# Optimization experiments

Measured on AMD Instinct MI355X. Metric: run time of the kernel, lower is better.

The kernel has to match this reference:

```python
import jax, jax.numpy as jnp
import numpy as np

B, N, D = 4, 512, 128
TAU = 0.5
EPS = 1e-9

def setup_inputs() -> dict:
    key = jax.random.key(0)
    ks = jax.random.split(key, 6)
    sc = 0.05  # weight scale for numerical sanity
    return {
        "entity_states": jax.random.normal(ks[0], (B, N, D), dtype=jnp.float32),
        "Wp": jax.random.normal(ks[1], (D, D), dtype=jnp.float32) * sc,
        "bp": jnp.zeros((D,), dtype=jnp.float32),
        "edge_logits": jax.random.normal(ks[2], (N, N), dtype=jnp.float32),
        "W1": jax.random.normal(ks[3], (2 * D, D), dtype=jnp.float32) * sc,
        "b1": jnp.zeros((D,), dtype=jnp.float32),
        "W2": jax.random.normal(ks[4], (D, D), dtype=jnp.float32) * sc,
        "b2": jnp.zeros((D,), dtype=jnp.float32),
        "u_noise": jax.random.uniform(ks[5], (N, N), dtype=jnp.float32),
    }

def reference(entity_states, Wp, bp, edge_logits, W1, b1, W2, b2, u_noise):
    b, n, d = entity_states.shape
    # entity projection
    proj = entity_states @ Wp + bp  # (B,N,D)
    # gumbel-softmax adjacency (row-wise softmax over sources)
    g = -jnp.log(-jnp.log(u_noise + EPS) + EPS)
    A = jax.nn.softmax((edge_logits + g) / TAU, axis=-1)  # (N,N)
    # split concat-MLP first layer: combined = [source_j, target_i]
    W1_src, W1_tgt = W1[:d], W1[d:]
    s = proj @ W1_src  # (B,N,D) contribution of source j
    t = proj @ W1_tgt  # (B,N,D) contribution of target i
    # h[b,i,j,:] = relu(s[b,j] + t[b,i] + b1)
    h = jax.nn.relu(s[:, None, :, :] + t[:, :, None, :] + b1)  # (B,N,N,D)
    msg = h @ W2 + b2  # (B,N,N,D)
    # weighted aggregation over sources j with A[i,j]
    upd = jnp.einsum('ij,bijd->bid', A, msg)  # (B,N,D)
    next_state = entity_states + upd
    return next_state, jnp.broadcast_to(A, (b, n, n))
```

## Files before the change

### kernel.cpp

```cpp
#include <hip/hip_runtime.h>
#include <math.h>

#define Bv 4
#define Nv 512
#define Dv 128
#define BND (Bv*Nv*Dv)
#define NN  (Nv*Nv)
#define EPSv 1e-9f

__global__ __launch_bounds__(256) void k_gumbel_softmax(
    const float* __restrict__ edge_logits,
    const float* __restrict__ u_noise,
    float* __restrict__ A_out)
{
    __shared__ float sred[4];
    const int row = blockIdx.x;
    const int t = threadIdx.x;

    const float u0 = u_noise[row*Nv + t];
    const float u1 = u_noise[row*Nv + t + 256];
    const float g0 = -logf(-logf(u0 + EPSv) + EPSv);
    const float g1 = -logf(-logf(u1 + EPSv) + EPSv);
    const float z0 = (edge_logits[row*Nv + t]       + g0) * 2.0f;
    const float z1 = (edge_logits[row*Nv + t + 256] + g1) * 2.0f;

    float m = fmaxf(z0, z1);
    #pragma unroll
    for (int off = 32; off >= 1; off >>= 1)
        m = fmaxf(m, __shfl_xor(m, off, 64));
    if ((t & 63) == 0) sred[t >> 6] = m;
    __syncthreads();
    m = fmaxf(fmaxf(sred[0], sred[1]), fmaxf(sred[2], sred[3]));

    const float e0 = expf(z0 - m);
    const float e1 = expf(z1 - m);
    float ssum = e0 + e1;
    #pragma unroll
    for (int off = 32; off >= 1; off >>= 1)
        ssum += __shfl_xor(ssum, off, 64);
    __syncthreads();
    if ((t & 63) == 0) sred[t >> 6] = ssum;
    __syncthreads();
    const float inv = 1.0f / (sred[0] + sred[1] + sred[2] + sred[3]);

    const float a0 = e0 * inv;
    const float a1 = e1 * inv;
    #pragma unroll
    for (int bb = 0; bb < Bv; ++bb) {
        A_out[bb*NN + row*Nv + t]       = a0;
        A_out[bb*NN + row*Nv + t + 256] = a1;
    }
}

__global__ __launch_bounds__(256) void k_proj_st(
    const float* __restrict__ ES, const float* __restrict__ Wp,
    const float* __restrict__ bp, const float* __restrict__ W1,
    const float* __restrict__ b1,
    float* __restrict__ s_out, float* __restrict__ t_out)
{
    __shared__ float es[8][Dv];
    __shared__ float pr[8][Dv];
    const int row0 = blockIdx.x * 8;
    const int t = threadIdx.x;
    const int c  = t & 127;
    const int rg = t >> 7;

    for (int idx = t; idx < 8*Dv; idx += 256)
        es[idx >> 7][idx & 127] = ES[(row0 + (idx >> 7))*Dv + (idx & 127)];
    __syncthreads();

    {
        float acc[4];
        const float bpc = bp[c];
        #pragma unroll
        for (int r = 0; r < 4; ++r) acc[r] = bpc;
        for (int k = 0; k < Dv; ++k) {
            const float w = Wp[k*Dv + c];
            #pragma unroll
            for (int r = 0; r < 4; ++r)
                acc[r] = fmaf(es[rg*4 + r][k], w, acc[r]);
        }
        #pragma unroll
        for (int r = 0; r < 4; ++r) pr[rg*4 + r][c] = acc[r];
    }
    __syncthreads();

    float sacc[4], tacc[4];
    const float b1c = b1[c];
    #pragma unroll
    for (int r = 0; r < 4; ++r) { sacc[r] = b1c; tacc[r] = 0.0f; }
    for (int k = 0; k < Dv; ++k) {
        const float ws_ = W1[k*Dv + c];
        const float wt_ = W1[(Dv + k)*Dv + c];
        #pragma unroll
        for (int r = 0; r < 4; ++r) {
            const float pv = pr[rg*4 + r][k];
            sacc[r] = fmaf(pv, ws_, sacc[r]);
            tacc[r] = fmaf(pv, wt_, tacc[r]);
        }
    }
    #pragma unroll
    for (int r = 0; r < 4; ++r) {
        const int row = row0 + rg*4 + r;
        s_out[row*Dv + c] = sacc[r];
        t_out[row*Dv + c] = tacc[r];
    }
}

__global__ __launch_bounds__(256) void k_aggregate(
    const float* __restrict__ s_buf, const float* __restrict__ t_buf,
    const float* __restrict__ A, float* __restrict__ hsum)
{
    const int JT = 64;
    __shared__ float sj[JT][Dv];
    const int b  = blockIdx.y;
    const int i0 = blockIdx.x * 4;
    const int t  = threadIdx.x;
    const int d  = t & 127;
    const int g  = __builtin_amdgcn_readfirstlane(t >> 7);
    const int ia = i0 + g*2;
    const int ib = ia + 1;

    const float tv0 = t_buf[(b*Nv + ia)*Dv + d];
    const float tv1 = t_buf[(b*Nv + ib)*Dv + d];
    const float* __restrict__ Ar0 = A + ia*Nv;
    const float* __restrict__ Ar1 = A + ib*Nv;

    float acc0 = 0.0f, acc1 = 0.0f;
    for (int jt = 0; jt < Nv; jt += JT) {
        __syncthreads();
        const float4* __restrict__ src = (const float4*)(s_buf + (b*Nv + jt)*Dv);
        float4* dst = (float4*)(&sj[0][0]);
        #pragma unroll
        for (int u = 0; u < 8; ++u)
            dst[t + u*256] = src[t + u*256];
        __syncthreads();
        #pragma unroll 4
        for (int j = 0; j < JT; ++j) {
            const float a0 = Ar0[jt + j];
            const float a1 = Ar1[jt + j];
            const float sv = sj[j][d];
            acc0 = fmaf(a0, fmaxf(sv + tv0, 0.0f), acc0);
            acc1 = fmaf(a1, fmaxf(sv + tv1, 0.0f), acc1);
        }
    }
    hsum[(b*Nv + ia)*Dv + d] = acc0;
    hsum[(b*Nv + ib)*Dv + d] = acc1;
}

__global__ __launch_bounds__(256) void k_final(
    const float* __restrict__ ES, const float* __restrict__ hsum,
    const float* __restrict__ W2, const float* __restrict__ b2,
    float* __restrict__ out)
{
    __shared__ float hs[8][Dv];
    const int row0 = blockIdx.x * 8;
    const int t = threadIdx.x;
    const int c  = t & 127;
    const int rg = t >> 7;

    for (int idx = t; idx < 8*Dv; idx += 256)
        hs[idx >> 7][idx & 127] = hsum[(row0 + (idx >> 7))*Dv + (idx & 127)];
    __syncthreads();

    float acc[4];
    const float b2c = b2[c];
    #pragma unroll
    for (int r = 0; r < 4; ++r) acc[r] = b2c;
    for (int k = 0; k < Dv; ++k) {
        const float w = W2[k*Dv + c];
        #pragma unroll
        for (int r = 0; r < 4; ++r)
            acc[r] = fmaf(hs[rg*4 + r][k], w, acc[r]);
    }
    #pragma unroll
    for (int r = 0; r < 4; ++r) {
        const int row = row0 + rg*4 + r;
        out[row*Dv + c] = ES[row*Dv + c] + acc[r];
    }
}

extern "C" void kernel_launch(void* const* d_in, const int* in_sizes, int n_in,
                              void* d_out, int out_size, void* d_ws, size_t ws_size,
                              hipStream_t stream) {
    (void)in_sizes; (void)n_in; (void)out_size; (void)ws_size;
    const float* ES = (const float*)d_in[0];
    const float* Wp = (const float*)d_in[1];
    const float* bp = (const float*)d_in[2];
    const float* EL = (const float*)d_in[3];
    const float* W1 = (const float*)d_in[4];
    const float* b1 = (const float*)d_in[5];
    const float* W2 = (const float*)d_in[6];
    const float* b2 = (const float*)d_in[7];
    const float* UN = (const float*)d_in[8];

    float* out   = (float*)d_out;
    float* A_out = out + BND;

    float* s_buf = (float*)d_ws;
    float* t_buf = s_buf + BND;
    float* h_buf = t_buf + BND;

    k_gumbel_softmax<<<Nv, 256, 0, stream>>>(EL, UN, A_out);
    k_proj_st<<<(Bv*Nv)/8, 256, 0, stream>>>(ES, Wp, bp, W1, b1, s_buf, t_buf);
    k_aggregate<<<dim3(Nv/4, Bv), 256, 0, stream>>>(s_buf, t_buf, A_out, h_buf);
    k_final<<<(Bv*Nv)/8, 256, 0, stream>>>(ES, h_buf, W2, b2, out);
}
```

Measured before the change: 122.4 us.

## Fuse gumbel-softmax and W2 projection into aggregation kernel

The gumbel-softmax is computed inside the aggregation kernel, one wave per row, with results kept in LDS and also written to the batched A output. The final W2 projection and residual add are done in the same kernel from LDS. This drops two launches and the hsum round trip through global memory. In exchange, each batch block recomputes the softmax for its rows (4x redundant log/exp work). Unroll pragmas are also added to the projection loops.

```diff
diff --git a/kernel.cpp b/kernel.cpp
--- a/kernel.cpp
+++ b/kernel.cpp
@@ -8,51 +8,7 @@
 #define NN  (Nv*Nv)
 #define EPSv 1e-9f
 
-__global__ __launch_bounds__(256) void k_gumbel_softmax(
-    const float* __restrict__ edge_logits,
-    const float* __restrict__ u_noise,
-    float* __restrict__ A_out)
-{
-    __shared__ float sred[4];
-    const int row = blockIdx.x;
-    const int t = threadIdx.x;
-
-    const float u0 = u_noise[row*Nv + t];
-    const float u1 = u_noise[row*Nv + t + 256];
-    const float g0 = -logf(-logf(u0 + EPSv) + EPSv);
-    const float g1 = -logf(-logf(u1 + EPSv) + EPSv);
-    const float z0 = (edge_logits[row*Nv + t]       + g0) * 2.0f;
-    const float z1 = (edge_logits[row*Nv + t + 256] + g1) * 2.0f;
-
-    float m = fmaxf(z0, z1);
-    #pragma unroll
-    for (int off = 32; off >= 1; off >>= 1)
-        m = fmaxf(m, __shfl_xor(m, off, 64));
-    if ((t & 63) == 0) sred[t >> 6] = m;
-    __syncthreads();
-    m = fmaxf(fmaxf(sred[0], sred[1]), fmaxf(sred[2], sred[3]));
-
-    const float e0 = expf(z0 - m);
-    const float e1 = expf(z1 - m);
-    float ssum = e0 + e1;
-    #pragma unroll
-    for (int off = 32; off >= 1; off >>= 1)
-        ssum += __shfl_xor(ssum, off, 64);
-    __syncthreads();
-    if ((t & 63) == 0) sred[t >> 6] = ssum;
-    __syncthreads();
-    const float inv = 1.0f / (sred[0] + sred[1] + sred[2] + sred[3]);
-
-    const float a0 = e0 * inv;
-    const float a1 = e1 * inv;
-    #pragma unroll
-    for (int bb = 0; bb < Bv; ++bb) {
-        A_out[bb*NN + row*Nv + t]       = a0;
-        A_out[bb*NN + row*Nv + t + 256] = a1;
-    }
-}
-
-__global__ __launch_bounds__(256) void k_proj_st(
+__global__ __launch_bounds__(256) void k_prep(
     const float* __restrict__ ES, const float* __restrict__ Wp,
     const float* __restrict__ bp, const float* __restrict__ W1,
     const float* __restrict__ b1,
@@ -74,6 +30,7 @@
         const float bpc = bp[c];
         #pragma unroll
         for (int r = 0; r < 4; ++r) acc[r] = bpc;
+        #pragma unroll 8
         for (int k = 0; k < Dv; ++k) {
             const float w = Wp[k*Dv + c];
             #pragma unroll
@@ -89,6 +46,7 @@
     const float b1c = b1[c];
     #pragma unroll
     for (int r = 0; r < 4; ++r) { sacc[r] = b1c; tacc[r] = 0.0f; }
+    #pragma unroll 8
     for (int k = 0; k < Dv; ++k) {
         const float ws_ = W1[k*Dv + c];
         const float wt_ = W1[(Dv + k)*Dv + c];
@@ -107,24 +65,61 @@
     }
 }
 
-__global__ __launch_bounds__(256) void k_aggregate(
+__global__ __launch_bounds__(256) void k_main(
     const float* __restrict__ s_buf, const float* __restrict__ t_buf,
-    const float* __restrict__ A, float* __restrict__ hsum)
+    const float* __restrict__ EL, const float* __restrict__ UN,
+    const float* __restrict__ ES, const float* __restrict__ W2,
+    const float* __restrict__ b2,
+    float* __restrict__ out, float* __restrict__ A_out)
 {
     const int JT = 64;
     __shared__ float sj[JT][Dv];
+    __shared__ float A_lds[4][Nv];
+    const int i0 = blockIdx.x * 4;
     const int b  = blockIdx.y;
-    const int i0 = blockIdx.x * 4;
     const int t  = threadIdx.x;
-    const int d  = t & 127;
-    const int g  = __builtin_amdgcn_readfirstlane(t >> 7);
-    const int ia = i0 + g*2;
+
+    {
+        const int w = t >> 6;
+        const int l = t & 63;
+        const int i = i0 + w;
+        float z[8], e[8];
+        float m = -1e30f;
+        #pragma unroll
+        for (int m8 = 0; m8 < 8; ++m8) {
+            const int c = l + 64*m8;
+            const float u = UN[i*Nv + c];
+            const float g = -logf(-logf(u + EPSv) + EPSv);
+            z[m8] = (EL[i*Nv + c] + g) * 2.0f;
+            m = fmaxf(m, z[m8]);
+        }
+        #pragma unroll
+        for (int off = 32; off >= 1; off >>= 1)
+            m = fmaxf(m, __shfl_xor(m, off, 64));
+        float ssum = 0.0f;
+        #pragma unroll
+        for (int m8 = 0; m8 < 8; ++m8) { e[m8] = expf(z[m8] - m); ssum += e[m8]; }
+        #pragma unroll
+        for (int off = 32; off >= 1; off >>= 1)
+            ssum += __shfl_xor(ssum, off, 64);
+        const float inv = 1.0f / ssum;
+        #pragma unroll
+        for (int m8 = 0; m8 < 8; ++m8) {
+            const int c = l + 64*m8;
+            const float a = e[m8] * inv;
+            A_lds[w][c] = a;
+            A_out[b*NN + i*Nv + c] = a;
+        }
+    }
+
+    const int d = t & 127;
+    const int g = __builtin_amdgcn_readfirstlane(t >> 7);
+    const int r0 = g*2;
+    const int ia = i0 + r0;
     const int ib = ia + 1;
 
     const float tv0 = t_buf[(b*Nv + ia)*Dv + d];
     const float tv1 = t_buf[(b*Nv + ib)*Dv + d];
-    const float* __restrict__ Ar0 = A + ia*Nv;
-    const float* __restrict__ Ar1 = A + ib*Nv;
 
     float acc0 = 0.0f, acc1 = 0.0f;
     for (int jt = 0; jt < Nv; jt += JT) {
@@ -137,47 +132,32 @@
         __syncthreads();
         #pragma unroll 4
         for (int j = 0; j < JT; ++j) {
-            const float a0 = Ar0[jt + j];
-            const float a1 = Ar1[jt + j];
+            const float a0 = A_lds[r0][jt + j];
+            const float a1 = A_lds[r0+1][jt + j];
             const float sv = sj[j][d];
             acc0 = fmaf(a0, fmaxf(sv + tv0, 0.0f), acc0);
             acc1 = fmaf(a1, fmaxf(sv + tv1, 0.0f), acc1);
         }
     }
-    hsum[(b*Nv + ia)*Dv + d] = acc0;
-    hsum[(b*Nv + ib)*Dv + d] = acc1;
-}
 
-__global__ __launch_bounds__(256) void k_final(
-    const float* __restrict__ ES, const float* __restrict__ hsum,
-    const float* __restrict__ W2, const float* __restrict__ b2,
-    float* __restrict__ out)
-{
-    __shared__ float hs[8][Dv];
-    const int row0 = blockIdx.x * 8;
-    const int t = threadIdx.x;
+    __syncthreads();
+    sj[r0][d]   = acc0;
+    sj[r0+1][d] = acc1;
+    __syncthreads();
+
     const int c  = t & 127;
     const int rg = t >> 7;
-
-    for (int idx = t; idx < 8*Dv; idx += 256)
-        hs[idx >> 7][idx & 127] = hsum[(row0 + (idx >> 7))*Dv + (idx & 127)];
-    __syncthreads();
-
-    float acc[4];
-    const float b2c = b2[c];
-    #pragma unroll
-    for (int r = 0; r < 4; ++r) acc[r] = b2c;
+    float o0 = b2[c], o1 = b2[c];
+    #pragma unroll 8
     for (int k = 0; k < Dv; ++k) {
-        const float w = W2[k*Dv + c];
-        #pragma unroll
-        for (int r = 0; r < 4; ++r)
-            acc[r] = fmaf(hs[rg*4 + r][k], w, acc[r]);
+        const float w2 = W2[k*Dv + c];
+        o0 = fmaf(sj[rg*2][k],   w2, o0);
+        o1 = fmaf(sj[rg*2+1][k], w2, o1);
     }
-    #pragma unroll
-    for (int r = 0; r < 4; ++r) {
-        const int row = row0 + rg*4 + r;
-        out[row*Dv + c] = ES[row*Dv + c] + acc[r];
-    }
+    const int ro0 = (b*Nv + i0 + rg*2)*Dv + c;
+    const int ro1 = ro0 + Dv;
+    out[ro0] = ES[ro0] + o0;
+    out[ro1] = ES[ro1] + o1;
 }
 
 extern "C" void kernel_launch(void* const* d_in, const int* in_sizes, int n_in,
@@ -199,10 +179,8 @@
 
     float* s_buf = (float*)d_ws;
     float* t_buf = s_buf + BND;
-    float* h_buf = t_buf + BND;
 
-    k_gumbel_softmax<<<Nv, 256, 0, stream>>>(EL, UN, A_out);
-    k_proj_st<<<(Bv*Nv)/8, 256, 0, stream>>>(ES, Wp, bp, W1, b1, s_buf, t_buf);
-    k_aggregate<<<dim3(Nv/4, Bv), 256, 0, stream>>>(s_buf, t_buf, A_out, h_buf);
-    k_final<<<(Bv*Nv)/8, 256, 0, stream>>>(ES, h_buf, W2, b2, out);
+    k_prep<<<(Bv*Nv)/8, 256, 0, stream>>>(ES, Wp, bp, W1, b1, s_buf, t_buf);
+    k_main<<<dim3(Nv/4, Bv), 256, 0, stream>>>(s_buf, t_buf, EL, UN, ES, W2, b2,
+                                               out, A_out);
 }
```

New measurement: 110.6 us. -9.6%, faster.

## Fuse kernels into prep and main stages, folding W2 projection into aggregation

Applied to the files above, without the earlier changes.

Merges the Gumbel-softmax and projection kernels into one prep kernel of 512 blocks (each handles one softmax row and four projection rows). It also folds the final W2 matmul and residual add into the aggregation kernel, reusing its shared memory to hold the per-row sums, which removes the hsum round trip and two launches. The aggregation tile grows from 64 to 128 source rows, halving the barrier-separated load phases but doubling shared memory per block, which may reduce occupancy.

```diff
diff --git a/kernel.cpp b/kernel.cpp
--- a/kernel.cpp
+++ b/kernel.cpp
@@ -8,131 +8,128 @@
 #define NN  (Nv*Nv)
 #define EPSv 1e-9f
 
-__global__ __launch_bounds__(256) void k_gumbel_softmax(
-    const float* __restrict__ edge_logits,
-    const float* __restrict__ u_noise,
+typedef float f2 __attribute__((ext_vector_type(2)));
+
+__global__ __launch_bounds__(256) void k_prep(
+    const float* __restrict__ ES, const float* __restrict__ Wp,
+    const float* __restrict__ bp, const float* __restrict__ W1,
+    const float* __restrict__ b1, const float* __restrict__ EL,
+    const float* __restrict__ UN,
+    float* __restrict__ s_out, float* __restrict__ t_out,
     float* __restrict__ A_out)
 {
+    __shared__ float es[4][Dv];
+    __shared__ float pr[4][Dv];
     __shared__ float sred[4];
-    const int row = blockIdx.x;
-    const int t = threadIdx.x;
+    const int bi = blockIdx.x;
+    const int t  = threadIdx.x;
 
-    const float u0 = u_noise[row*Nv + t];
-    const float u1 = u_noise[row*Nv + t + 256];
-    const float g0 = -logf(-logf(u0 + EPSv) + EPSv);
-    const float g1 = -logf(-logf(u1 + EPSv) + EPSv);
-    const float z0 = (edge_logits[row*Nv + t]       + g0) * 2.0f;
-    const float z1 = (edge_logits[row*Nv + t + 256] + g1) * 2.0f;
+    {
+        const int row = bi;
+        const float u0 = UN[row*Nv + t];
+        const float u1 = UN[row*Nv + t + 256];
+        const float g0 = -logf(-logf(u0 + EPSv) + EPSv);
+        const float g1 = -logf(-logf(u1 + EPSv) + EPSv);
+        const float z0 = (EL[row*Nv + t]       + g0) * 2.0f;
+        const float z1 = (EL[row*Nv + t + 256] + g1) * 2.0f;
 
-    float m = fmaxf(z0, z1);
-    #pragma unroll
-    for (int off = 32; off >= 1; off >>= 1)
-        m = fmaxf(m, __shfl_xor(m, off, 64));
-    if ((t & 63) == 0) sred[t >> 6] = m;
-    __syncthreads();
-    m = fmaxf(fmaxf(sred[0], sred[1]), fmaxf(sred[2], sred[3]));
+        float m = fmaxf(z0, z1);
+        #pragma unroll
+        for (int off = 32; off >= 1; off >>= 1)
+            m = fmaxf(m, __shfl_xor(m, off, 64));
+        if ((t & 63) == 0) sred[t >> 6] = m;
+        __syncthreads();
+        m = fmaxf(fmaxf(sred[0], sred[1]), fmaxf(sred[2], sred[3]));
 
-    const float e0 = expf(z0 - m);
-    const float e1 = expf(z1 - m);
-    float ssum = e0 + e1;
-    #pragma unroll
-    for (int off = 32; off >= 1; off >>= 1)
-        ssum += __shfl_xor(ssum, off, 64);
-    __syncthreads();
-    if ((t & 63) == 0) sred[t >> 6] = ssum;
-    __syncthreads();
-    const float inv = 1.0f / (sred[0] + sred[1] + sred[2] + sred[3]);
+        const float e0 = expf(z0 - m);
+        const float e1 = expf(z1 - m);
+        float ssum = e0 + e1;
+        #pragma unroll
+        for (int off = 32; off >= 1; off >>= 1)
+            ssum += __shfl_xor(ssum, off, 64);
+        __syncthreads();
+        if ((t & 63) == 0) sred[t >> 6] = ssum;
+        __syncthreads();
+        const float inv = 1.0f / (sred[0] + sred[1] + sred[2] + sred[3]);
+        const float a0 = e0 * inv;
+        const float a1 = e1 * inv;
+        #pragma unroll
+        for (int bb = 0; bb < Bv; ++bb) {
+            A_out[bb*NN + row*Nv + t]       = a0;
+            A_out[bb*NN + row*Nv + t + 256] = a1;
+        }
+    }
 
-    const float a0 = e0 * inv;
-    const float a1 = e1 * inv;
-    #pragma unroll
-    for (int bb = 0; bb < Bv; ++bb) {
-        A_out[bb*NN + row*Nv + t]       = a0;
-        A_out[bb*NN + row*Nv + t + 256] = a1;
-    }
-}
-
-__global__ __launch_bounds__(256) void k_proj_st(
-    const float* __restrict__ ES, const float* __restrict__ Wp,
-    const float* __restrict__ bp, const float* __restrict__ W1,
-    const float* __restrict__ b1,
-    float* __restrict__ s_out, float* __restrict__ t_out)
-{
-    __shared__ float es[8][Dv];
-    __shared__ float pr[8][Dv];
-    const int row0 = blockIdx.x * 8;
-    const int t = threadIdx.x;
+    const int row0 = bi * 4;
     const int c  = t & 127;
     const int rg = t >> 7;
 
-    for (int idx = t; idx < 8*Dv; idx += 256)
+    for (int idx = t; idx < 4*Dv; idx += 256)
         es[idx >> 7][idx & 127] = ES[(row0 + (idx >> 7))*Dv + (idx & 127)];
     __syncthreads();
 
     {
-        float acc[4];
+        float acc[2];
         const float bpc = bp[c];
-        #pragma unroll
-        for (int r = 0; r < 4; ++r) acc[r] = bpc;
+        acc[0] = bpc; acc[1] = bpc;
+        #pragma unroll 8
         for (int k = 0; k < Dv; ++k) {
             const float w = Wp[k*Dv + c];
-            #pragma unroll
-            for (int r = 0; r < 4; ++r)
-                acc[r] = fmaf(es[rg*4 + r][k], w, acc[r]);
+            acc[0] = fmaf(es[rg*2][k],   w, acc[0]);
+            acc[1] = fmaf(es[rg*2+1][k], w, acc[1]);
         }
-        #pragma unroll
-        for (int r = 0; r < 4; ++r) pr[rg*4 + r][c] = acc[r];
+        pr[rg*2][c]   = acc[0];
+        pr[rg*2+1][c] = acc[1];
     }
     __syncthreads();
 
-    float sacc[4], tacc[4];
-    const float b1c = b1[c];
-    #pragma unroll
-    for (int r = 0; r < 4; ++r) { sacc[r] = b1c; tacc[r] = 0.0f; }
+    float sacc0 = b1[c], sacc1 = sacc0, tacc0 = 0.0f, tacc1 = 0.0f;
+    #pragma unroll 8
     for (int k = 0; k < Dv; ++k) {
         const float ws_ = W1[k*Dv + c];
         const float wt_ = W1[(Dv + k)*Dv + c];
-        #pragma unroll
-        for (int r = 0; r < 4; ++r) {
-            const float pv = pr[rg*4 + r][k];
-            sacc[r] = fmaf(pv, ws_, sacc[r]);
-            tacc[r] = fmaf(pv, wt_, tacc[r]);
-        }
+        const float p0 = pr[rg*2][k];
+        const float p1 = pr[rg*2+1][k];
+        sacc0 = fmaf(p0, ws_, sacc0);
+        sacc1 = fmaf(p1, ws_, sacc1);
+        tacc0 = fmaf(p0, wt_, tacc0);
+        tacc1 = fmaf(p1, wt_, tacc1);
     }
-    #pragma unroll
-    for (int r = 0; r < 4; ++r) {
-        const int row = row0 + rg*4 + r;
-        s_out[row*Dv + c] = sacc[r];
-        t_out[row*Dv + c] = tacc[r];
-    }
+    const int ra = (row0 + rg*2)*Dv + c;
+    s_out[ra]      = sacc0;
+    s_out[ra + Dv] = sacc1;
+    t_out[ra]      = tacc0;
+    t_out[ra + Dv] = tacc1;
 }
 
-__global__ __launch_bounds__(256) void k_aggregate(
+__global__ __launch_bounds__(256) void k_main(
     const float* __restrict__ s_buf, const float* __restrict__ t_buf,
-    const float* __restrict__ A, float* __restrict__ hsum)
+    const float* __restrict__ A0,    const float* __restrict__ ES,
+    const float* __restrict__ W2,    const float* __restrict__ b2,
+    float* __restrict__ out)
 {
-    const int JT = 64;
+    const int JT = 128;
     __shared__ float sj[JT][Dv];
+    const int i0 = blockIdx.x * 4;
     const int b  = blockIdx.y;
-    const int i0 = blockIdx.x * 4;
     const int t  = threadIdx.x;
     const int d  = t & 127;
-    const int g  = __builtin_amdgcn_readfirstlane(t >> 7);
-    const int ia = i0 + g*2;
-    const int ib = ia + 1;
+    const int p  = __builtin_amdgcn_readfirstlane(t >> 7);
+    const int ia = i0 + 2*p;
 
-    const float tv0 = t_buf[(b*Nv + ia)*Dv + d];
-    const float tv1 = t_buf[(b*Nv + ib)*Dv + d];
-    const float* __restrict__ Ar0 = A + ia*Nv;
-    const float* __restrict__ Ar1 = A + ib*Nv;
+    f2 tv;
+    tv.x = t_buf[(b*Nv + ia)*Dv + d];
+    tv.y = t_buf[(b*Nv + ia + 1)*Dv + d];
+    const float* __restrict__ Ar0 = A0 + ia*Nv;
+    const float* __restrict__ Ar1 = A0 + (ia + 1)*Nv;
 
-    float acc0 = 0.0f, acc1 = 0.0f;
+    f2 acc; acc.x = 0.0f; acc.y = 0.0f;
     for (int jt = 0; jt < Nv; jt += JT) {
         __syncthreads();
         const float4* __restrict__ src = (const float4*)(s_buf + (b*Nv + jt)*Dv);
         float4* dst = (float4*)(&sj[0][0]);
         #pragma unroll
-        for (int u = 0; u < 8; ++u)
+        for (int u = 0; u < 16; ++u)
             dst[t + u*256] = src[t + u*256];
         __syncthreads();
         #pragma unroll 4
@@ -140,44 +137,30 @@
             const float a0 = Ar0[jt + j];
             const float a1 = Ar1[jt + j];
             const float sv = sj[j][d];
-            acc0 = fmaf(a0, fmaxf(sv + tv0, 0.0f), acc0);
-            acc1 = fmaf(a1, fmaxf(sv + tv1, 0.0f), acc1);
+            f2 z; z.x = sv + tv.x; z.y = sv + tv.y;
+            f2 r; r.x = fmaxf(z.x, 0.0f); r.y = fmaxf(z.y, 0.0f);
+            acc.x = fmaf(a0, r.x, acc.x);
+            acc.y = fmaf(a1, r.y, acc.y);
         }
     }
-    hsum[(b*Nv + ia)*Dv + d] = acc0;
-    hsum[(b*Nv + ib)*Dv + d] = acc1;
-}
 
-__global__ __launch_bounds__(256) void k_final(
-    const float* __restrict__ ES, const float* __restrict__ hsum,
-    const float* __restrict__ W2, const float* __restrict__ b2,
-    float* __restrict__ out)
-{
-    __shared__ float hs[8][Dv];
-    const int row0 = blockIdx.x * 8;
-    const int t = threadIdx.x;
+    __syncthreads();
+    sj[2*p][d]     = acc.x;
+    sj[2*p + 1][d] = acc.y;
+    __syncthreads();
+
     const int c  = t & 127;
     const int rg = t >> 7;
-
-    for (int idx = t; idx < 8*Dv; idx += 256)
-        hs[idx >> 7][idx & 127] = hsum[(row0 + (idx >> 7))*Dv + (idx & 127)];
-    __syncthreads();
-
-    float acc[4];
-    const float b2c = b2[c];
-    #pragma unroll
-    for (int r = 0; r < 4; ++r) acc[r] = b2c;
+    float o0 = b2[c], o1 = o0;
+    #pragma unroll 8
     for (int k = 0; k < Dv; ++k) {
-        const float w = W2[k*Dv + c];
-        #pragma unroll
-        for (int r = 0; r < 4; ++r)
-            acc[r] = fmaf(hs[rg*4 + r][k], w, acc[r]);
+        const float w2 = W2[k*Dv + c];
+        o0 = fmaf(sj[rg*2][k],   w2, o0);
+        o1 = fmaf(sj[rg*2+1][k], w2, o1);
     }
-    #pragma unroll
-    for (int r = 0; r < 4; ++r) {
-        const int row = row0 + rg*4 + r;
-        out[row*Dv + c] = ES[row*Dv + c] + acc[r];
-    }
+    const int ro0 = (b*Nv + i0 + rg*2)*Dv + c;
+    out[ro0]      = ES[ro0]      + o0;
+    out[ro0 + Dv] = ES[ro0 + Dv] + o1;
 }
 
 extern "C" void kernel_launch(void* const* d_in, const int* in_sizes, int n_in,
@@ -199,10 +182,9 @@
 
     float* s_buf = (float*)d_ws;
     float* t_buf = s_buf + BND;
-    float* h_buf = t_buf + BND;
 
-    k_gumbel_softmax<<<Nv, 256, 0, stream>>>(EL, UN, A_out);
-    k_proj_st<<<(Bv*Nv)/8, 256, 0, stream>>>(ES, Wp, bp, W1, b1, s_buf, t_buf);
-    k_aggregate<<<dim3(Nv/4, Bv), 256, 0, stream>>>(s_buf, t_buf, A_out, h_buf);
-    k_final<<<(Bv*Nv)/8, 256, 0, stream>>>(ES, h_buf, W2, b2, out);
+    k_prep<<<512, 256, 0, stream>>>(ES, Wp, bp, W1, b1, EL, UN,
+                                    s_buf, t_buf, A_out);
+    k_main<<<dim3(Nv/4, Bv), 256, 0, stream>>>(s_buf, t_buf, A_out, ES, W2, b2,
+                                               out);
 }
```

Measured after the change: 114.0 us. 1.07x faster.
